# Optimization experiments

Hardware: AMD Instinct MI355X
Metric: run time of the kernel (lower is better)

The kernel has to match this reference:

```python
import jax, jax.numpy as jnp
import numpy as np

EPS_BN = 1e-5
EPS_LN = 1e-5


def _conv1d(x, w, b, pad):
    # x: (B, Cin, L), w: (Cout, Cin, K)
    y = jax.lax.conv_general_dilated(x, w, window_strides=(1,), padding=[(pad, pad)],
                                     dimension_numbers=('NCH', 'OIH', 'NCH'))
    return y + b[None, :, None]


def _bn_eval(x, g, b, m, v):
    return (x - m[None, :, None]) * (g / jnp.sqrt(v + EPS_BN))[None, :, None] + b[None, :, None]


def _maxpool2(x):
    B, C, L = x.shape
    return x.reshape(B, C, L // 2, 2).max(-1)


def _wavelet(x, t, s, w):
    # x: (B, In); t, s, w: (Out, In); mexican_hat wavelet
    z = (x[:, None, :] - t[None]) / (s + 1e-8)  # (B, Out, In)
    wav = (1.0 - z * z) * jnp.exp(-0.5 * z * z)
    return jnp.einsum('boi,oi->bo', wav, w)


def _ln(x, g, b):
    m = x.mean(-1, keepdims=True)
    v = ((x - m) ** 2).mean(-1, keepdims=True)
    return (x - m) / jnp.sqrt(v + EPS_LN) * g + b


def setup_inputs() -> dict:
    key = jax.random.key(0)
    ks = iter(jax.random.split(key, 40))
    B, L = 1024, 1024
    R = 64                 # repr_dim
    KIN = 128 * (R // 4)   # 2048 = conv stem flattened features
    d = {}
    d['x'] = jax.random.normal(next(ks), (B, 1, L), jnp.float32)
    for i, (ci, co, k) in enumerate([(1, 32, 7), (32, 64, 5), (64, 128, 3)], 1):
        fan = ci * k
        d[f'conv{i}_w'] = jax.random.normal(next(ks), (co, ci, k), jnp.float32) / np.sqrt(fan)
        d[f'conv{i}_b'] = jnp.zeros((co,), jnp.float32)
        d[f'bn{i}_g'] = jnp.ones((co,), jnp.float32)
        d[f'bn{i}_b'] = jnp.zeros((co,), jnp.float32)
        d[f'bn{i}_m'] = jax.random.normal(next(ks), (co,), jnp.float32) * 0.1
        d[f'bn{i}_v'] = jax.random.uniform(next(ks), (co,), jnp.float32, 0.5, 1.5)
    for i, fin in enumerate([KIN, R, R], 1):
        d[f'wl{i}_t'] = jax.random.uniform(next(ks), (R, fin), jnp.float32, -1.0, 1.0)
        d[f'wl{i}_s'] = jax.random.uniform(next(ks), (R, fin), jnp.float32, 0.1, 1.0)
        d[f'wl{i}_w'] = jax.random.normal(next(ks), (R, fin), jnp.float32) / np.sqrt(fin)
        d[f'ln{i}_g'] = jnp.ones((R,), jnp.float32)
        d[f'ln{i}_b'] = jnp.zeros((R,), jnp.float32)
    return d


def _forward(x, p):
    h = _conv1d(x, p['conv1_w'], p['conv1_b'], 3)
    h = jax.nn.gelu(_bn_eval(h, p['bn1_g'], p['bn1_b'], p['bn1_m'], p['bn1_v']), approximate=False)
    h = _maxpool2(h)
    h = _conv1d(h, p['conv2_w'], p['conv2_b'], 2)
    h = jax.nn.gelu(_bn_eval(h, p['bn2_g'], p['bn2_b'], p['bn2_m'], p['bn2_v']), approximate=False)
    h = _maxpool2(h)
    h = _conv1d(h, p['conv3_w'], p['conv3_b'], 1)
    h = jax.nn.gelu(_bn_eval(h, p['bn3_g'], p['bn3_b'], p['bn3_m'], p['bn3_v']), approximate=False)
    # AdaptiveAvgPool1d(16): L=256 splits evenly into 16 bins of 16
    B, C, L = h.shape
    h = h.reshape(B, C, 16, L // 16).mean(-1)
    feat = h.reshape(B, -1)  # (B, 2048)
    for i in (1, 2, 3):
        feat = _ln(jax.nn.silu(_wavelet(feat, p[f'wl{i}_t'], p[f'wl{i}_s'], p[f'wl{i}_w'])),
                   p[f'ln{i}_g'], p[f'ln{i}_b'])
    return feat  # (B, 64)


def reference(x, conv1_w, conv1_b, bn1_g, bn1_b, bn1_m, bn1_v,
              conv2_w, conv2_b, bn2_g, bn2_b, bn2_m, bn2_v,
              conv3_w, conv3_b, bn3_g, bn3_b, bn3_m, bn3_v,
              wl1_t, wl1_s, wl1_w, ln1_g, ln1_b,
              wl2_t, wl2_s, wl2_w, ln2_g, ln2_b,
              wl3_t, wl3_s, wl3_w, ln3_g, ln3_b):
    p = dict(locals())
    p.pop('x')
    return _forward(x, p)
```

## Files before the change

### kernel.cpp

```cpp
#include <hip/hip_runtime.h>
#include <hip/hip_bf16.h>
#include <math.h>

#define WS_W2H   0
#define WS_W2L   5120
#define WS_W3H   10240
#define WS_W3L   23040
#define WS_A1    35840
#define WS_C1    35872
#define WS_A2    35904
#define WS_C2    35968
#define WS_A3    36032
#define WS_C3    36160
#define WS_T1T   36288
#define WS_IS1T  167360
#define WS_WW1T  298432
#define WS_T2T   429504
#define WS_IS2T  433600
#define WS_WW2T  437696
#define WS_T3T   441792
#define WS_IS3T  445888
#define WS_WW3T  449984
#define WS_FEAT  454080

typedef _Float16 f16x8 __attribute__((ext_vector_type(8)));
typedef float    f32x4 __attribute__((ext_vector_type(4)));

struct InPtrs { const float* p[34]; };

__device__ __forceinline__ float gelu_fast(float x) {
    float z  = 0.70710678118654752f * x;
    float az = fabsf(z);
    float t  = __builtin_amdgcn_rcpf(fmaf(0.3275911f, az, 1.0f));
    float p  = fmaf(1.061405429f, t, -1.453152027f);
    p = fmaf(p, t, 1.421413741f);
    p = fmaf(p, t, -0.284496736f);
    p = fmaf(p, t, 0.254829592f);
    p = p * t;
    float e  = __expf(-z * z);
    float erf_abs = fmaf(-p, e, 1.0f);
    float erfv = copysignf(erf_abs, z);
    return 0.5f * x * (1.0f + erfv);
}

__global__ __launch_bounds__(256) void prep_kernel(InPtrs in, float* __restrict__ ws) {
    int idx = blockIdx.x * 256 + threadIdx.x;
    if (idx >= 453856) return;
    if (idx < 10240) {
        int co = idx / 160; int kk = idx - co * 160;
        int tap = kk >> 5, ci = kk & 31;
        float val = in.p[7][co * 160 + ci * 5 + tap];
        _Float16 hi = (_Float16)val;
        ((_Float16*)(ws + WS_W2H))[co * 160 + kk] = hi;
        ((_Float16*)(ws + WS_W2L))[co * 160 + kk] = (_Float16)(val - (float)hi);
    } else if (idx < 35840) {
        int n = idx - 10240;
        int co = n / 200; int k = n - co * 200;
        float val = 0.0f;
        if (k < 192) { int ci = k & 63; int tap = k >> 6; val = in.p[13][co * 192 + ci * 3 + tap]; }
        _Float16 hi = (_Float16)val;
        ((_Float16*)(ws + WS_W3H))[co * 200 + k] = hi;
        ((_Float16*)(ws + WS_W3L))[co * 200 + k] = (_Float16)(val - (float)hi);
    } else if (idx < 36064) {
        int n = idx - 35840;
        int ch, offA, offC; const float *cb, *g, *bb, *m, *v;
        if (n < 32)      { ch = n;      cb = in.p[2];  g = in.p[3];  bb = in.p[4];  m = in.p[5];  v = in.p[6];  offA = WS_A1; offC = WS_C1; }
        else if (n < 96) { ch = n - 32; cb = in.p[8];  g = in.p[9];  bb = in.p[10]; m = in.p[11]; v = in.p[12]; offA = WS_A2; offC = WS_C2; }
        else             { ch = n - 96; cb = in.p[14]; g = in.p[15]; bb = in.p[16]; m = in.p[17]; v = in.p[18]; offA = WS_A3; offC = WS_C3; }
        float A = g[ch] * rsqrtf(v[ch] + 1e-5f);
        ws[offA + ch] = A;
        ws[offC + ch] = (cb[ch] - m[ch]) * A + bb[ch];
    } else if (idx < 429280) {
        int n = idx - 36064;
        int arr = n / 131072; int m = n - arr * 131072;
        int o = m >> 11; int i = m & 2047;
        float val = in.p[19 + arr][o * 2048 + i];
        if (arr == 1) val = 1.0f / (val + 1e-8f);
        int base = (arr == 0) ? WS_T1T : (arr == 1) ? WS_IS1T : WS_WW1T;
        ws[base + i * 64 + o] = val;
    } else {
        int n = idx - 429280;
        int layer = n / 12288; int m = n - layer * 12288;
        int arr = m / 4096; int mm = m - arr * 4096;
        int o = mm >> 6; int i = mm & 63;
        float val = in.p[(layer == 0 ? 24 : 29) + arr][o * 64 + i];
        if (arr == 1) val = 1.0f / (val + 1e-8f);
        int base;
        if (layer == 0) base = (arr == 0) ? WS_T2T : (arr == 1) ? WS_IS2T : WS_WW2T;
        else            base = (arr == 0) ? WS_T3T : (arr == 1) ? WS_IS3T : WS_WW3T;
        ws[base + i * 64 + o] = val;
    }
}

__global__ __launch_bounds__(256) void kconv_kernel(const float* __restrict__ x,
                                                    const float* __restrict__ w1,
                                                    const float* __restrict__ ws,
                                                    const _Float16* __restrict__ w3h,
                                                    const _Float16* __restrict__ w3l,
                                                    float* __restrict__ feat) {
    __shared__ float xs[560];
    __shared__ float w1s[224];
    __shared__ float a1s[32], c1s[32], a2s[64], c2s[64];
    __shared__ __align__(16) _Float16 U[2 * 276 * 40];

    _Float16* h1h = U;
    _Float16* h1l = U + 276 * 40;

    int t = threadIdx.x;
    int b = blockIdx.x >> 1, q = blockIdx.x & 1;

    for (int j = t; j < 558; j += 256) {
        int gx = 512 * q - 11 + j;
        xs[j] = (gx >= 0 && gx < 1024) ? x[b * 1024 + gx] : 0.0f;
    }
    if (t < 224) w1s[t] = w1[t];
    if (t < 32) { a1s[t] = ws[WS_A1 + t]; c1s[t] = ws[WS_C1 + t]; }
    if (t < 64) { a2s[t] = ws[WS_A2 + t]; c2s[t] = ws[WS_C2 + t]; }
    __syncthreads();

    for (int item = t; item < 276 * 32; item += 256) {
        int r = item >> 5, ci = item & 31;
        int hp = 256 * q - 4 + r;
        float val = 0.0f;
        if (hp >= 0 && hp < 512) {
            float d0 = 0.0f, d1 = 0.0f;
            #pragma unroll
            for (int k = 0; k < 7; ++k) {
                float w = w1s[ci * 7 + k];
                d0 += w * xs[2 * r + k];
                d1 += w * xs[2 * r + k + 1];
            }
            float A = a1s[ci], C = c1s[ci];
            val = fmaxf(gelu_fast(d0 * A + C), gelu_fast(d1 * A + C));
        }
        _Float16 hi = (_Float16)val;
        h1h[r * 40 + ci] = hi;
        h1l[r * 40 + ci] = (_Float16)(val - (float)hi);
    }
    __syncthreads();

    int w = t >> 6, lane = t & 63;
    int m = lane & 15, quad = lane >> 4;

    const _Float16* w2h = (const _Float16*)(ws + WS_W2H);
    const _Float16* w2l = (const _Float16*)(ws + WS_W2L);
    f32x4 acc[5][4] = {};

    #pragma unroll
    for (int s = 0; s < 5; ++s) {
        f16x8 bh[4], bl[4];
        #pragma unroll
        for (int tc = 0; tc < 4; ++tc) {
            int off = (16 * tc + m) * 160 + 32 * s + quad * 8;
            bh[tc] = *(const f16x8*)(w2h + off);
            bl[tc] = *(const f16x8*)(w2l + off);
        }
        #pragma unroll
        for (int i = 0; i < 5; ++i) {
            if (i == 4 && w != 0) continue;
            int fr = (i < 4) ? (4 * i + w) : 16;
            f16x8 ah = *(const f16x8*)(&h1h[(16 * fr + m + s) * 40 + quad * 8]);
            f16x8 al = *(const f16x8*)(&h1l[(16 * fr + m + s) * 40 + quad * 8]);
            #pragma unroll
            for (int tc = 0; tc < 4; ++tc) {
                acc[i][tc] = __builtin_amdgcn_mfma_f32_16x16x32_f16(ah, bh[tc], acc[i][tc], 0, 0, 0);
                acc[i][tc] = __builtin_amdgcn_mfma_f32_16x16x32_f16(al, bh[tc], acc[i][tc], 0, 0, 0);
                acc[i][tc] = __builtin_amdgcn_mfma_f32_16x16x32_f16(ah, bl[tc], acc[i][tc], 0, 0, 0);
            }
        }
    }
    __syncthreads();

    _Float16* h2h = U;
    _Float16* h2l = U + 130 * 72;
    if (q == 0 && t < 64) { h2h[0 * 72 + t]   = (_Float16)0.f; h2l[0 * 72 + t]   = (_Float16)0.f; }
    if (q == 1 && t < 64) { h2h[129 * 72 + t] = (_Float16)0.f; h2l[129 * 72 + t] = (_Float16)0.f; }

    #pragma unroll
    for (int i = 0; i < 5; ++i) {
        if (i == 4 && w != 0) continue;
        int fr = (i < 4) ? (4 * i + w) : 16;
        #pragma unroll
        for (int tc = 0; tc < 4; ++tc) {
            int co = 16 * tc + m;
            float A2 = a2s[co], C2 = c2s[co];
            float g0 = gelu_fast(acc[i][tc][0] * A2 + C2);
            float g1 = gelu_fast(acc[i][tc][1] * A2 + C2);
            float g2 = gelu_fast(acc[i][tc][2] * A2 + C2);
            float g3 = gelu_fast(acc[i][tc][3] * A2 + C2);
            float p0 = fmaxf(g0, g1), p1 = fmaxf(g2, g3);
            int ll0 = 8 * fr + 2 * quad;
            int lg0 = 128 * q - 1 + ll0;
            if (ll0 < 130 && (unsigned)lg0 < 256u) {
                _Float16 h0 = (_Float16)p0;
                h2h[ll0 * 72 + co] = h0;
                h2l[ll0 * 72 + co] = (_Float16)(p0 - (float)h0);
            }
            int ll1 = ll0 + 1, lg1 = lg0 + 1;
            if (ll1 < 130 && (unsigned)lg1 < 256u) {
                _Float16 h1v = (_Float16)p1;
                h2h[ll1 * 72 + co] = h1v;
                h2l[ll1 * 72 + co] = (_Float16)(p1 - (float)h1v);
            }
        }
    }
    __syncthreads();

    int wr = w >> 1, wc = w & 1;
    f32x4 acc2[4][4] = {};
    size_t boff = (size_t)(wc * 64 + m) * 200 + quad * 8;

    #pragma unroll
    for (int s = 0; s < 6; ++s) {
        int kbase = s * 32;
        int k = kbase + quad * 8;
        int koff = k >> 6, ci = k & 63;
        f16x8 ah[4], al[4], bh[4], bl[4];
        #pragma unroll
        for (int tr = 0; tr < 4; ++tr) {
            int row = 64 * wr + 16 * tr + m;
            ah[tr] = *(const f16x8*)(&h2h[(row + koff) * 72 + ci]);
            al[tr] = *(const f16x8*)(&h2l[(row + koff) * 72 + ci]);
        }
        #pragma unroll
        for (int tc = 0; tc < 4; ++tc) {
            bh[tc] = *(const f16x8*)(w3h + boff + 16 * tc * 200 + kbase);
            bl[tc] = *(const f16x8*)(w3l + boff + 16 * tc * 200 + kbase);
        }
        #pragma unroll
        for (int tr = 0; tr < 4; ++tr)
            #pragma unroll
            for (int tc = 0; tc < 4; ++tc) {
                acc2[tr][tc] = __builtin_amdgcn_mfma_f32_16x16x32_f16(ah[tr], bh[tc], acc2[tr][tc], 0, 0, 0);
                acc2[tr][tc] = __builtin_amdgcn_mfma_f32_16x16x32_f16(al[tr], bh[tc], acc2[tr][tc], 0, 0, 0);
                acc2[tr][tc] = __builtin_amdgcn_mfma_f32_16x16x32_f16(ah[tr], bl[tc], acc2[tr][tc], 0, 0, 0);
            }
    }

    #pragma unroll
    for (int tc = 0; tc < 4; ++tc) {
        int co = 64 * wc + 16 * tc + m;
        float A3 = ws[WS_A3 + co], C3 = ws[WS_C3 + co];
        #pragma unroll
        for (int tr = 0; tr < 4; ++tr) {
            float s = 0.0f;
            #pragma unroll
            for (int r = 0; r < 4; ++r)
                s += gelu_fast(acc2[tr][tc][r] * A3 + C3);
            s += __shfl_xor(s, 16, 64);
            s += __shfl_xor(s, 32, 64);
            if (quad == 0) {
                int bin = 8 * q + 4 * wr + tr;
                feat[(size_t)b * 2048 + co * 16 + bin] = s * 0.0625f;
            }
        }
    }
}

__device__ __forceinline__ float wave_sum(float v) {
    #pragma unroll
    for (int off = 32; off > 0; off >>= 1) v += __shfl_xor(v, off, 64);
    return v;
}
__device__ __forceinline__ float silu_f(float v) {
    return v / (1.0f + __expf(-v));
}

__global__ __launch_bounds__(1024) void k4_kernel(const float* __restrict__ ws,
        const float* __restrict__ ln1g, const float* __restrict__ ln1b,
        const float* __restrict__ ln2g, const float* __restrict__ ln2b,
        const float* __restrict__ ln3g, const float* __restrict__ ln3b,
        float* __restrict__ out) {
    __shared__ __align__(16) float fs[4 * 2048];
    __shared__ float red[16 * 256];

    int t = threadIdx.x;
    int b0 = blockIdx.x * 4;
    const float* feat = ws + WS_FEAT;
    {
        const float4* src = (const float4*)(feat + (size_t)b0 * 2048);
        float4* dst = (float4*)fs;
        for (int i = t; i < 2048; i += 1024) dst[i] = src[i];
    }
    __syncthreads();

    int o = t & 63, grp = t >> 6;
    const float* t1t  = ws + WS_T1T;
    const float* is1t = ws + WS_IS1T;
    const float* w1t  = ws + WS_WW1T;
    float acc0 = 0.0f, acc1 = 0.0f, acc2 = 0.0f, acc3 = 0.0f;
    int i0 = grp * 128;
    for (int i = i0; i < i0 + 128; ++i) {
        float tv = t1t[i * 64 + o], sv = is1t[i * 64 + o], wv = w1t[i * 64 + o];
        float z, z2;
        z = (fs[i] - tv) * sv;        z2 = z * z; acc0 += (1.0f - z2) * __expf(-0.5f * z2) * wv;
        z = (fs[2048 + i] - tv) * sv; z2 = z * z; acc1 += (1.0f - z2) * __expf(-0.5f * z2) * wv;
        z = (fs[4096 + i] - tv) * sv; z2 = z * z; acc2 += (1.0f - z2) * __expf(-0.5f * z2) * wv;
        z = (fs[6144 + i] - tv) * sv; z2 = z * z; acc3 += (1.0f - z2) * __expf(-0.5f * z2) * wv;
    }
    red[grp * 256 + 0 * 64 + o] = acc0;
    red[grp * 256 + 1 * 64 + o] = acc1;
    red[grp * 256 + 2 * 64 + o] = acc2;
    red[grp * 256 + 3 * 64 + o] = acc3;
    __syncthreads();

    if (grp < 4) {
        int w = grp;
        float y = 0.0f;
        #pragma unroll
        for (int j = 0; j < 16; ++j) y += red[j * 256 + w * 64 + o];

        y = silu_f(y);
        float m = wave_sum(y) * 0.015625f;
        float d = y - m;
        float var = wave_sum(d * d) * 0.015625f;
        float yn = d * rsqrtf(var + 1e-5f) * ln1g[o] + ln1b[o];

        {
            const float* t2t  = ws + WS_T2T;
            const float* is2t = ws + WS_IS2T;
            const float* w2t  = ws + WS_WW2T;
            float a = 0.0f;
            for (int i = 0; i < 64; ++i) {
                float xi = __shfl(yn, i, 64);
                float tv = t2t[i * 64 + o], sv = is2t[i * 64 + o], wv = w2t[i * 64 + o];
                float z = (xi - tv) * sv, z2 = z * z;
                a += (1.0f - z2) * __expf(-0.5f * z2) * wv;
            }
            float y2 = silu_f(a);
            float m2 = wave_sum(y2) * 0.015625f;
            float d2 = y2 - m2;
            float v2 = wave_sum(d2 * d2) * 0.015625f;
            yn = d2 * rsqrtf(v2 + 1e-5f) * ln2g[o] + ln2b[o];
        }
        {
            const float* t3t  = ws + WS_T3T;
            const float* is3t = ws + WS_IS3T;
            const float* w3t  = ws + WS_WW3T;
            float a = 0.0f;
            for (int i = 0; i < 64; ++i) {
                float xi = __shfl(yn, i, 64);
                float tv = t3t[i * 64 + o], sv = is3t[i * 64 + o], wv = w3t[i * 64 + o];
                float z = (xi - tv) * sv, z2 = z * z;
                a += (1.0f - z2) * __expf(-0.5f * z2) * wv;
            }
            float y3 = silu_f(a);
            float m3 = wave_sum(y3) * 0.015625f;
            float d3 = y3 - m3;
            float v3 = wave_sum(d3 * d3) * 0.015625f;
            yn = d3 * rsqrtf(v3 + 1e-5f) * ln3g[o] + ln3b[o];
        }
        out[((size_t)b0 + w) * 64 + o] = yn;
    }
}

extern "C" void kernel_launch(void* const* d_in, const int* in_sizes, int n_in,
                              void* d_out, int out_size, void* d_ws, size_t ws_size,
                              hipStream_t stream) {
    float* ws = (float*)d_ws;
    InPtrs ip;
    for (int i = 0; i < 34; ++i) ip.p[i] = (const float*)d_in[i];

    prep_kernel<<<1774, 256, 0, stream>>>(ip, ws);
    kconv_kernel<<<2048, 256, 0, stream>>>((const float*)d_in[0], (const float*)d_in[1],
                                           ws,
                                           (const _Float16*)(ws + WS_W3H),
                                           (const _Float16*)(ws + WS_W3L),
                                           ws + WS_FEAT);
    k4_kernel<<<256, 1024, 0, stream>>>(ws,
        (const float*)d_in[22], (const float*)d_in[23],
        (const float*)d_in[27], (const float*)d_in[28],
        (const float*)d_in[32], (const float*)d_in[33],
        (float*)d_out);
}
```

Baseline: 318.9 us.

## Drop activation low-part fp16 split and vectorize conv1 with register tiling

Activations for the conv2 and conv3 MFMA GEMMs are now stored only as a single fp16 value instead of a hi/lo split, which removes one third of the MFMAs, half the LDS activation traffic and half the shared-memory footprint. Weights keep their hi/lo split. Conv1 is restructured so each thread computes four output rows for one channel using float4 loads of the input window held in registers. This lowers accuracy of the activations to plain fp16, which may affect tolerance.

```diff
diff --git a/kernel.cpp b/kernel.cpp
--- a/kernel.cpp
+++ b/kernel.cpp
@@ -98,18 +98,17 @@
                                                     const _Float16* __restrict__ w3h,
                                                     const _Float16* __restrict__ w3l,
                                                     float* __restrict__ feat) {
-    __shared__ float xs[560];
+    __shared__ __align__(16) float xs[560];
     __shared__ float w1s[224];
     __shared__ float a1s[32], c1s[32], a2s[64], c2s[64];
-    __shared__ __align__(16) _Float16 U[2 * 276 * 40];
-
-    _Float16* h1h = U;
-    _Float16* h1l = U + 276 * 40;
+    __shared__ __align__(16) _Float16 U[276 * 40];
+
+    _Float16* h1s = U;
 
     int t = threadIdx.x;
     int b = blockIdx.x >> 1, q = blockIdx.x & 1;
 
-    for (int j = t; j < 558; j += 256) {
+    for (int j = t; j < 560; j += 256) {
         int gx = 512 * q - 11 + j;
         xs[j] = (gx >= 0 && gx < 1024) ? x[b * 1024 + gx] : 0.0f;
     }
@@ -118,24 +117,31 @@
     if (t < 64) { a2s[t] = ws[WS_A2 + t]; c2s[t] = ws[WS_C2 + t]; }
     __syncthreads();
 
-    for (int item = t; item < 276 * 32; item += 256) {
-        int r = item >> 5, ci = item & 31;
-        int hp = 256 * q - 4 + r;
-        float val = 0.0f;
-        if (hp >= 0 && hp < 512) {
-            float d0 = 0.0f, d1 = 0.0f;
-            #pragma unroll
-            for (int k = 0; k < 7; ++k) {
-                float w = w1s[ci * 7 + k];
-                d0 += w * xs[2 * r + k];
-                d1 += w * xs[2 * r + k + 1];
-            }
-            float A = a1s[ci], C = c1s[ci];
-            val = fmaxf(gelu_fast(d0 * A + C), gelu_fast(d1 * A + C));
-        }
-        _Float16 hi = (_Float16)val;
-        h1h[r * 40 + ci] = hi;
-        h1l[r * 40 + ci] = (_Float16)(val - (float)hi);
+    for (int item = t; item < 32 * 69; item += 256) {
+        int ci = item / 69, rq = item - ci * 69;
+        const float4* xp = (const float4*)(xs + 8 * rq);
+        float4 X0 = xp[0], X1 = xp[1], X2 = xp[2], X3 = xp[3];
+        float f[16] = {X0.x, X0.y, X0.z, X0.w, X1.x, X1.y, X1.z, X1.w,
+                       X2.x, X2.y, X2.z, X2.w, X3.x, X3.y, X3.z, X3.w};
+        float wk0 = w1s[ci * 7],     wk1 = w1s[ci * 7 + 1], wk2 = w1s[ci * 7 + 2];
+        float wk3 = w1s[ci * 7 + 3], wk4 = w1s[ci * 7 + 4], wk5 = w1s[ci * 7 + 5];
+        float wk6 = w1s[ci * 7 + 6];
+        float A = a1s[ci], C = c1s[ci];
+        #pragma unroll
+        for (int r4 = 0; r4 < 4; ++r4) {
+            int r = 4 * rq + r4;
+            int hp = 256 * q - 4 + r;
+            float val = 0.0f;
+            if ((unsigned)hp < 512u) {
+                int j = 2 * r4;
+                float d0 = f[j]*wk0 + f[j+1]*wk1 + f[j+2]*wk2 + f[j+3]*wk3
+                         + f[j+4]*wk4 + f[j+5]*wk5 + f[j+6]*wk6;
+                float d1 = f[j+1]*wk0 + f[j+2]*wk1 + f[j+3]*wk2 + f[j+4]*wk3
+                         + f[j+5]*wk4 + f[j+6]*wk5 + f[j+7]*wk6;
+                val = fmaxf(gelu_fast(fmaf(d0, A, C)), gelu_fast(fmaf(d1, A, C)));
+            }
+            h1s[r * 40 + ci] = (_Float16)val;
+        }
     }
     __syncthreads();
 
@@ -159,22 +165,19 @@
         for (int i = 0; i < 5; ++i) {
             if (i == 4 && w != 0) continue;
             int fr = (i < 4) ? (4 * i + w) : 16;
-            f16x8 ah = *(const f16x8*)(&h1h[(16 * fr + m + s) * 40 + quad * 8]);
-            f16x8 al = *(const f16x8*)(&h1l[(16 * fr + m + s) * 40 + quad * 8]);
+            f16x8 ah = *(const f16x8*)(&h1s[(16 * fr + m + s) * 40 + quad * 8]);
             #pragma unroll
             for (int tc = 0; tc < 4; ++tc) {
                 acc[i][tc] = __builtin_amdgcn_mfma_f32_16x16x32_f16(ah, bh[tc], acc[i][tc], 0, 0, 0);
-                acc[i][tc] = __builtin_amdgcn_mfma_f32_16x16x32_f16(al, bh[tc], acc[i][tc], 0, 0, 0);
                 acc[i][tc] = __builtin_amdgcn_mfma_f32_16x16x32_f16(ah, bl[tc], acc[i][tc], 0, 0, 0);
             }
         }
     }
     __syncthreads();
 
-    _Float16* h2h = U;
-    _Float16* h2l = U + 130 * 72;
-    if (q == 0 && t < 64) { h2h[0 * 72 + t]   = (_Float16)0.f; h2l[0 * 72 + t]   = (_Float16)0.f; }
-    if (q == 1 && t < 64) { h2h[129 * 72 + t] = (_Float16)0.f; h2l[129 * 72 + t] = (_Float16)0.f; }
+    _Float16* h2s = U;
+    if (q == 0 && t < 64) h2s[0 * 72 + t]   = (_Float16)0.f;
+    if (q == 1 && t < 64) h2s[129 * 72 + t] = (_Float16)0.f;
 
     #pragma unroll
     for (int i = 0; i < 5; ++i) {
@@ -184,24 +187,16 @@
         for (int tc = 0; tc < 4; ++tc) {
             int co = 16 * tc + m;
             float A2 = a2s[co], C2 = c2s[co];
-            float g0 = gelu_fast(acc[i][tc][0] * A2 + C2);
-            float g1 = gelu_fast(acc[i][tc][1] * A2 + C2);
-            float g2 = gelu_fast(acc[i][tc][2] * A2 + C2);
-            float g3 = gelu_fast(acc[i][tc][3] * A2 + C2);
+            float g0 = gelu_fast(fmaf(acc[i][tc][0], A2, C2));
+            float g1 = gelu_fast(fmaf(acc[i][tc][1], A2, C2));
+            float g2 = gelu_fast(fmaf(acc[i][tc][2], A2, C2));
+            float g3 = gelu_fast(fmaf(acc[i][tc][3], A2, C2));
             float p0 = fmaxf(g0, g1), p1 = fmaxf(g2, g3);
             int ll0 = 8 * fr + 2 * quad;
             int lg0 = 128 * q - 1 + ll0;
-            if (ll0 < 130 && (unsigned)lg0 < 256u) {
-                _Float16 h0 = (_Float16)p0;
-                h2h[ll0 * 72 + co] = h0;
-                h2l[ll0 * 72 + co] = (_Float16)(p0 - (float)h0);
-            }
+            if (ll0 < 130 && (unsigned)lg0 < 256u) h2s[ll0 * 72 + co] = (_Float16)p0;
             int ll1 = ll0 + 1, lg1 = lg0 + 1;
-            if (ll1 < 130 && (unsigned)lg1 < 256u) {
-                _Float16 h1v = (_Float16)p1;
-                h2h[ll1 * 72 + co] = h1v;
-                h2l[ll1 * 72 + co] = (_Float16)(p1 - (float)h1v);
-            }
+            if (ll1 < 130 && (unsigned)lg1 < 256u) h2s[ll1 * 72 + co] = (_Float16)p1;
         }
     }
     __syncthreads();
@@ -215,12 +210,11 @@
         int kbase = s * 32;
         int k = kbase + quad * 8;
         int koff = k >> 6, ci = k & 63;
-        f16x8 ah[4], al[4], bh[4], bl[4];
+        f16x8 ah[4], bh[4], bl[4];
         #pragma unroll
         for (int tr = 0; tr < 4; ++tr) {
             int row = 64 * wr + 16 * tr + m;
-            ah[tr] = *(const f16x8*)(&h2h[(row + koff) * 72 + ci]);
-            al[tr] = *(const f16x8*)(&h2l[(row + koff) * 72 + ci]);
+            ah[tr] = *(const f16x8*)(&h2s[(row + koff) * 72 + ci]);
         }
         #pragma unroll
         for (int tc = 0; tc < 4; ++tc) {
@@ -232,7 +226,6 @@
             #pragma unroll
             for (int tc = 0; tc < 4; ++tc) {
                 acc2[tr][tc] = __builtin_amdgcn_mfma_f32_16x16x32_f16(ah[tr], bh[tc], acc2[tr][tc], 0, 0, 0);
-                acc2[tr][tc] = __builtin_amdgcn_mfma_f32_16x16x32_f16(al[tr], bh[tc], acc2[tr][tc], 0, 0, 0);
                 acc2[tr][tc] = __builtin_amdgcn_mfma_f32_16x16x32_f16(ah[tr], bl[tc], acc2[tr][tc], 0, 0, 0);
             }
     }
@@ -246,7 +239,7 @@
             float s = 0.0f;
             #pragma unroll
             for (int r = 0; r < 4; ++r)
-                s += gelu_fast(acc2[tr][tc][r] * A3 + C3);
+                s += gelu_fast(fmaf(acc2[tr][tc][r], A3, C3));
             s += __shfl_xor(s, 16, 64);
             s += __shfl_xor(s, 32, 64);
             if (quad == 0) {
```

New measurement: 310.6 us. -2.6%, faster.
